# Performance work log

Hardware: AMD Instinct MI355X
Metric: run time of the kernel (lower is better)

## Reference

```python
import jax, jax.numpy as jnp
import numpy as np

B, M, D, DH, DV = 16384, 3, 2048, 1024, 512

def setup_inputs() -> dict:
    key = jax.random.key(0)
    kx, kq, kk, kv, kf = jax.random.split(key, 5)
    x = jax.random.normal(kx, (B, M, D), dtype=jnp.float32)
    # nn.Linear weights are [out, in]; q/k/v scaled by 1/32 as in __init__
    Wq = jax.random.normal(kq, (DH, D), dtype=jnp.float32) / 32.0
    Wk = jax.random.normal(kk, (DH, D), dtype=jnp.float32) / 32.0
    Wv = jax.random.normal(kv, (DV, D), dtype=jnp.float32) / 32.0
    Wfc = jax.random.normal(kf, (1, DV), dtype=jnp.float32)
    return {"x": x, "Wq": Wq, "Wk": Wk, "Wv": Wv, "Wfc": Wfc}

def reference(x, Wq, Wk, Wv, Wfc):
    # q,k: [B,M,DH]; v: [B,M,DV]
    q = jnp.einsum('bmd,hd->bmh', x, Wq)
    k = jnp.einsum('bmd,hd->bmh', x, Wk)
    v = jnp.einsum('bmd,vd->bmv', x, Wv)
    qk = jnp.einsum('bih,bjh->bij', q, k)          # [B,M,M]
    attn = jax.nn.softmax(qk, axis=2)
    attn = jnp.sum(attn, axis=1) / M               # [B,M] (sum over queries, avg)
    z = jnp.einsum('bm,bmv->bv', attn, v)          # [B,DV]
    return z @ Wfc.T                               # [B,1]
```

## Files before the change

kernel.cpp:

```cpp
#include <hip/hip_runtime.h>
#include <hip/hip_bf16.h>
#include <stdint.h>
#include <stddef.h>

#define B_   16384
#define M_   3
#define D_   2048
#define DH_  1024
#define DV_  512
#define ROWS (B_ * M_)
#define NOUT (2 * DH_)

typedef _Float16 f16;
typedef f16   f16x8 __attribute__((ext_vector_type(8)));
typedef float f32x4 __attribute__((ext_vector_type(4)));

__device__ __forceinline__ void async16(const void* g, void* l) {
  __builtin_amdgcn_global_load_lds(
      (const __attribute__((address_space(1))) void*)g,
      (__attribute__((address_space(3))) void*)l, 16, 0, 0);
}

__global__ void k_wvf(const float* __restrict__ Wv, const float* __restrict__ Wfc,
                      float* __restrict__ wvf) {
  int d = blockIdx.x * 256 + threadIdx.x;
  float acc = 0.f;
  for (int v = 0; v < DV_; ++v) acc += Wfc[v] * Wv[(size_t)v * D_ + d];
  wvf[d] = acc;
}

__global__ void k_castw(const float* __restrict__ Wq, const float* __restrict__ Wk,
                        f16* __restrict__ Wh) {
  int t = blockIdx.x * 256 + threadIdx.x;
  int idx = t * 8;
  int j = idx >> 11;
  int d = idx & (D_ - 1);
  const float* src = (j < DH_) ? (Wq + (size_t)j * D_ + d)
                               : (Wk + (size_t)(j - DH_) * D_ + d);
  f32x4 a = *(const f32x4*)src;
  f32x4 b = *(const f32x4*)(src + 4);
  f16x8 h;
  h[0] = (f16)a[0]; h[1] = (f16)a[1]; h[2] = (f16)a[2]; h[3] = (f16)a[3];
  h[4] = (f16)b[0]; h[5] = (f16)b[1]; h[6] = (f16)b[2]; h[7] = (f16)b[3];
  *(f16x8*)(Wh + (size_t)idx) = h;
}

__global__ void k_prep(const float* __restrict__ x, const float* __restrict__ wvf,
                       f16* __restrict__ Xh, float* __restrict__ vf) {
  int row = blockIdx.x;
  int tid = threadIdx.x;
  const float* xr = x + (size_t)row * D_ + tid * 8;
  f32x4 a = *(const f32x4*)xr;
  f32x4 b = *(const f32x4*)(xr + 4);
  const float* wp = wvf + tid * 8;
  f32x4 wa = *(const f32x4*)wp;
  f32x4 wb = *(const f32x4*)(wp + 4);
  f16x8 h;
  h[0] = (f16)a[0]; h[1] = (f16)a[1]; h[2] = (f16)a[2]; h[3] = (f16)a[3];
  h[4] = (f16)b[0]; h[5] = (f16)b[1]; h[6] = (f16)b[2]; h[7] = (f16)b[3];
  *(f16x8*)(Xh + (size_t)row * D_ + tid * 8) = h;
  float acc = a[0]*wa[0] + a[1]*wa[1] + a[2]*wa[2] + a[3]*wa[3]
            + b[0]*wb[0] + b[1]*wb[1] + b[2]*wb[2] + b[3]*wb[3];
  #pragma unroll
  for (int off = 1; off < 64; off <<= 1) acc += __shfl_xor(acc, off);
  __shared__ float red[4];
  if ((tid & 63) == 0) red[tid >> 6] = acc;
  __syncthreads();
  if (tid == 0) vf[row] = red[0] + red[1] + red[2] + red[3];
}

__global__ __launch_bounds__(256, 3) void k_gemm(const f16* __restrict__ Xh,
                                                 const f16* __restrict__ Wh,
                                                 f16* __restrict__ QK) {
  const int ct = blockIdx.x;
  const int rt = blockIdx.y;
  const int tid = threadIdx.x;
  const int w = tid >> 6, lane = tid & 63;
  const int wr = w >> 1, wc = w & 1;

  __shared__ __align__(16) f16 lds_a[128 * 32];
  __shared__ __align__(16) f16 lds_b[128 * 32];

  f32x4 acc[4][4] = {};

  const int srow = lane >> 2;
  const int scol = (lane & 3) * 8;
  const int q0 = w * 2, q1 = q0 + 1;

  const f16* gA0 = Xh + (size_t)(rt * 128 + q0 * 16 + srow) * D_ + scol;
  const f16* gA1 = Xh + (size_t)(rt * 128 + q1 * 16 + srow) * D_ + scol;
  const f16* gB0 = Wh + (size_t)(ct * 128 + q0 * 16 + srow) * D_ + scol;
  const f16* gB1 = Wh + (size_t)(ct * 128 + q1 * 16 + srow) * D_ + scol;

  f16* la0 = &lds_a[q0 * 512];
  f16* la1 = &lds_a[q1 * 512];
  f16* lb0 = &lds_b[q0 * 512];
  f16* lb1 = &lds_b[q1 * 512];

  const f16* fa = &lds_a[(size_t)(wr * 64 + (lane & 15)) * 32 + (lane >> 4) * 8];
  const f16* fb = &lds_b[(size_t)(wc * 64 + (lane & 15)) * 32 + (lane >> 4) * 8];

  for (int k0 = 0; k0 < D_; k0 += 32) {
    async16(gA0 + k0, la0);
    async16(gA1 + k0, la1);
    async16(gB0 + k0, lb0);
    async16(gB1 + k0, lb1);
    __syncthreads();
    f16x8 af[4], bf[4];
    #pragma unroll
    for (int i = 0; i < 4; ++i) af[i] = *(const f16x8*)(fa + i * 16 * 32);
    #pragma unroll
    for (int j = 0; j < 4; ++j) bf[j] = *(const f16x8*)(fb + j * 16 * 32);
    #pragma unroll
    for (int i = 0; i < 4; ++i)
      #pragma unroll
      for (int j = 0; j < 4; ++j)
        acc[i][j] = __builtin_amdgcn_mfma_f32_16x16x32_f16(af[i], bf[j], acc[i][j], 0, 0, 0);
    __syncthreads();
  }

  const int r0 = rt * 128 + wr * 64 + (lane >> 4) * 4;
  const int c0 = ct * 128 + wc * 64 + (lane & 15);
  #pragma unroll
  for (int i = 0; i < 4; ++i)
    #pragma unroll
    for (int j = 0; j < 4; ++j)
      #pragma unroll
      for (int r = 0; r < 4; ++r)
        QK[(size_t)(r0 + i * 16 + r) * NOUT + (c0 + j * 16)] = (f16)acc[i][j][r];
}

__global__ void k_attn(const f16* __restrict__ QK, const float* __restrict__ vf,
                       float* __restrict__ out) {
  int w = threadIdx.x >> 6, lane = threadIdx.x & 63;
  int b = blockIdx.x * 4 + w;
  const f16* base = QK + (size_t)b * M_ * NOUT;
  f16x8 q[3][2], k[3][2];
  #pragma unroll
  for (int i = 0; i < 3; ++i) {
    q[i][0] = *(const f16x8*)(base + i * NOUT + lane * 8);
    q[i][1] = *(const f16x8*)(base + i * NOUT + 512 + lane * 8);
    k[i][0] = *(const f16x8*)(base + i * NOUT + 1024 + lane * 8);
    k[i][1] = *(const f16x8*)(base + i * NOUT + 1536 + lane * 8);
  }
  float s[3][3];
  #pragma unroll
  for (int i = 0; i < 3; ++i)
    #pragma unroll
    for (int j = 0; j < 3; ++j) {
      float a = 0.f;
      #pragma unroll
      for (int c = 0; c < 2; ++c)
        #pragma unroll
        for (int t = 0; t < 8; ++t)
          a += (float)q[i][c][t] * (float)k[j][c][t];
      s[i][j] = a;
    }
  #pragma unroll
  for (int i = 0; i < 3; ++i)
    #pragma unroll
    for (int j = 0; j < 3; ++j)
      #pragma unroll
      for (int off = 1; off < 64; off <<= 1)
        s[i][j] += __shfl_xor(s[i][j], off);
  if (lane == 0) {
    float attn[3] = {0.f, 0.f, 0.f};
    #pragma unroll
    for (int i = 0; i < 3; ++i) {
      float m = fmaxf(s[i][0], fmaxf(s[i][1], s[i][2]));
      float e0 = expf(s[i][0] - m), e1 = expf(s[i][1] - m), e2 = expf(s[i][2] - m);
      float inv = 1.f / (e0 + e1 + e2);
      attn[0] += e0 * inv; attn[1] += e1 * inv; attn[2] += e2 * inv;
    }
    float o = attn[0] * vf[b * 3 + 0] + attn[1] * vf[b * 3 + 1] + attn[2] * vf[b * 3 + 2];
    out[b] = o * (1.f / 3.f);
  }
}

extern "C" void kernel_launch(void* const* d_in, const int* in_sizes, int n_in,
                              void* d_out, int out_size, void* d_ws, size_t ws_size,
                              hipStream_t stream) {
  const float* x   = (const float*)d_in[0];
  const float* Wq  = (const float*)d_in[1];
  const float* Wk  = (const float*)d_in[2];
  const float* Wv  = (const float*)d_in[3];
  const float* Wfc = (const float*)d_in[4];
  float* out = (float*)d_out;

  char* ws = (char*)d_ws;
  f16*   Xh  = (f16*)(ws);
  f16*   QK  = (f16*)(ws + 201326592ull);
  f16*   Wh  = (f16*)(ws + 402653184ull);
  float* wvf = (float*)(ws + 411041792ull);
  float* vf  = (float*)(ws + 411049984ull);

  k_wvf  <<<8,              256, 0, stream>>>(Wv, Wfc, wvf);
  k_castw<<<2048,           256, 0, stream>>>(Wq, Wk, Wh);
  k_prep <<<ROWS,           256, 0, stream>>>(x, wvf, Xh, vf);
  k_gemm <<<dim3(16, 384),  256, 0, stream>>>(Xh, Wh, QK);
  k_attn <<<B_ / 4,         256, 0, stream>>>(QK, vf, out);
}
```

Measured before the change: 1.086 ms.

## Swizzle GEMM LDS layout, raise occupancy, parallelize wvf and prep kernels

```diff
diff --git a/kernel.cpp b/kernel.cpp
--- a/kernel.cpp
+++ b/kernel.cpp
@@ -23,10 +23,22 @@
 
 __global__ void k_wvf(const float* __restrict__ Wv, const float* __restrict__ Wfc,
                       float* __restrict__ wvf) {
-  int d = blockIdx.x * 256 + threadIdx.x;
+  int dl = threadIdx.x & 31;
+  int vs = threadIdx.x >> 5;
+  int d = blockIdx.x * 32 + dl;
   float acc = 0.f;
-  for (int v = 0; v < DV_; ++v) acc += Wfc[v] * Wv[(size_t)v * D_ + d];
-  wvf[d] = acc;
+  #pragma unroll 8
+  for (int v = vs * 64; v < vs * 64 + 64; ++v)
+    acc += Wfc[v] * Wv[(size_t)v * D_ + d];
+  __shared__ float red[8][32];
+  red[vs][dl] = acc;
+  __syncthreads();
+  if (threadIdx.x < 32) {
+    float s = 0.f;
+    #pragma unroll
+    for (int i = 0; i < 8; ++i) s += red[i][threadIdx.x];
+    wvf[blockIdx.x * 32 + threadIdx.x] = s;
+  }
 }
 
 __global__ void k_castw(const float* __restrict__ Wq, const float* __restrict__ Wk,
@@ -47,29 +59,31 @@
 
 __global__ void k_prep(const float* __restrict__ x, const float* __restrict__ wvf,
                        f16* __restrict__ Xh, float* __restrict__ vf) {
-  int row = blockIdx.x;
-  int tid = threadIdx.x;
-  const float* xr = x + (size_t)row * D_ + tid * 8;
-  f32x4 a = *(const f32x4*)xr;
-  f32x4 b = *(const f32x4*)(xr + 4);
-  const float* wp = wvf + tid * 8;
-  f32x4 wa = *(const f32x4*)wp;
-  f32x4 wb = *(const f32x4*)(wp + 4);
-  f16x8 h;
-  h[0] = (f16)a[0]; h[1] = (f16)a[1]; h[2] = (f16)a[2]; h[3] = (f16)a[3];
-  h[4] = (f16)b[0]; h[5] = (f16)b[1]; h[6] = (f16)b[2]; h[7] = (f16)b[3];
-  *(f16x8*)(Xh + (size_t)row * D_ + tid * 8) = h;
-  float acc = a[0]*wa[0] + a[1]*wa[1] + a[2]*wa[2] + a[3]*wa[3]
-            + b[0]*wb[0] + b[1]*wb[1] + b[2]*wb[2] + b[3]*wb[3];
+  int w = threadIdx.x >> 6, lane = threadIdx.x & 63;
+  int row = blockIdx.x * 4 + w;
+  const float* xr = x + (size_t)row * D_;
+  f16* xo = Xh + (size_t)row * D_;
+  float acc = 0.f;
+  #pragma unroll
+  for (int p = 0; p < 4; ++p) {
+    int col = p * 512 + lane * 8;
+    f32x4 a = *(const f32x4*)(xr + col);
+    f32x4 b = *(const f32x4*)(xr + col + 4);
+    f32x4 wa = *(const f32x4*)(wvf + col);
+    f32x4 wb = *(const f32x4*)(wvf + col + 4);
+    f16x8 h;
+    h[0] = (f16)a[0]; h[1] = (f16)a[1]; h[2] = (f16)a[2]; h[3] = (f16)a[3];
+    h[4] = (f16)b[0]; h[5] = (f16)b[1]; h[6] = (f16)b[2]; h[7] = (f16)b[3];
+    *(f16x8*)(xo + col) = h;
+    acc += a[0]*wa[0] + a[1]*wa[1] + a[2]*wa[2] + a[3]*wa[3]
+         + b[0]*wb[0] + b[1]*wb[1] + b[2]*wb[2] + b[3]*wb[3];
+  }
   #pragma unroll
   for (int off = 1; off < 64; off <<= 1) acc += __shfl_xor(acc, off);
-  __shared__ float red[4];
-  if ((tid & 63) == 0) red[tid >> 6] = acc;
-  __syncthreads();
-  if (tid == 0) vf[row] = red[0] + red[1] + red[2] + red[3];
-}
-
-__global__ __launch_bounds__(256, 3) void k_gemm(const f16* __restrict__ Xh,
+  if (lane == 0) vf[row] = acc;
+}
+
+__global__ __launch_bounds__(256, 4) void k_gemm(const f16* __restrict__ Xh,
                                                  const f16* __restrict__ Wh,
                                                  f16* __restrict__ QK) {
   const int ct = blockIdx.x;
@@ -84,7 +98,8 @@
   f32x4 acc[4][4] = {};
 
   const int srow = lane >> 2;
-  const int scol = (lane & 3) * 8;
+  const int schunk = (lane & 3) ^ ((lane >> 3) & 3);
+  const int scol = schunk * 8;
   const int q0 = w * 2, q1 = q0 + 1;
 
   const f16* gA0 = Xh + (size_t)(rt * 128 + q0 * 16 + srow) * D_ + scol;
@@ -97,8 +112,10 @@
   f16* lb0 = &lds_b[q0 * 512];
   f16* lb1 = &lds_b[q1 * 512];
 
-  const f16* fa = &lds_a[(size_t)(wr * 64 + (lane & 15)) * 32 + (lane >> 4) * 8];
-  const f16* fb = &lds_b[(size_t)(wc * 64 + (lane & 15)) * 32 + (lane >> 4) * 8];
+  const int fr = lane & 15;
+  const int fq = (lane >> 4) ^ ((fr >> 1) & 3);
+  const f16* fa = &lds_a[(size_t)(wr * 64 + fr) * 32 + fq * 8];
+  const f16* fb = &lds_b[(size_t)(wc * 64 + fr) * 32 + fq * 8];
 
   for (int k0 = 0; k0 < D_; k0 += 32) {
     async16(gA0 + k0, la0);
@@ -194,9 +211,9 @@
   float* wvf = (float*)(ws + 411041792ull);
   float* vf  = (float*)(ws + 411049984ull);
 
-  k_wvf  <<<8,              256, 0, stream>>>(Wv, Wfc, wvf);
+  k_wvf  <<<64,             256, 0, stream>>>(Wv, Wfc, wvf);
   k_castw<<<2048,           256, 0, stream>>>(Wq, Wk, Wh);
-  k_prep <<<ROWS,           256, 0, stream>>>(x, wvf, Xh, vf);
+  k_prep <<<ROWS / 4,       256, 0, stream>>>(x, wvf, Xh, vf);
   k_gemm <<<dim3(16, 384),  256, 0, stream>>>(Xh, Wh, QK);
   k_attn <<<B_ / 4,         256, 0, stream>>>(QK, vf, out);
 }
```

After: 1.066 ms. Within noise of the previous version (-1.8%).
